# Performance work log

Hardware: AMD Instinct MI355X
Metric: run time of the kernel (lower is better)

The kernel has to match this reference:

```python
import jax, jax.numpy as jnp
import numpy as np

N_NODES = 50000
N_EDGES = 600000
CLASSIC_DIM = 128
GRAPH_OUTPUT_DIM = 96
NUM_RELATIONS = 4


def setup_inputs() -> dict:
    key = jax.random.key(0)
    ks = jax.random.split(key, 10)
    x = jax.random.normal(ks[0], (N_NODES, CLASSIC_DIM), dtype=jnp.float32)
    edge_index = jax.random.randint(ks[1], (2, N_EDGES), 0, N_NODES, dtype=jnp.int64)
    edge_type = jax.random.randint(ks[2], (N_EDGES,), 0, NUM_RELATIONS, dtype=jnp.int64)
    s1 = 1.0 / np.sqrt(CLASSIC_DIM)
    W_root1 = jax.random.normal(ks[3], (CLASSIC_DIM, CLASSIC_DIM), dtype=jnp.float32) * s1
    W_rel1 = jax.random.normal(ks[4], (NUM_RELATIONS, CLASSIC_DIM, CLASSIC_DIM), dtype=jnp.float32) * s1
    b1 = jnp.zeros((CLASSIC_DIM,), dtype=jnp.float32)
    W_root2 = jax.random.normal(ks[5], (CLASSIC_DIM, GRAPH_OUTPUT_DIM), dtype=jnp.float32) * s1
    W_rel2 = jax.random.normal(ks[6], (NUM_RELATIONS, CLASSIC_DIM, GRAPH_OUTPUT_DIM), dtype=jnp.float32) * s1
    b2 = jnp.zeros((GRAPH_OUTPUT_DIM,), dtype=jnp.float32)
    return {"classic_features": x, "edge_index": edge_index, "edge_type": edge_type,
            "W_root1": W_root1, "W_rel1": W_rel1, "b1": b1,
            "W_root2": W_root2, "W_rel2": W_rel2, "b2": b2}


def _rgcn_layer(x, edge_index, edge_type, W_root, W_rel, b):
    # RGCN: h_i = W_root x_i + b + sum_r (1/deg_{i,r}) * W_r * sum_{j in N_r(i)} x_j
    # Aggregate-then-transform (valid by linearity) to keep the matmul small.
    src, dst = edge_index[0], edge_index[1]
    msgs = x[src]  # [E, d_in] irregular gather
    out = x @ W_root + b
    n = x.shape[0]
    num_rel = W_rel.shape[0]
    for r in range(num_rel):  # small fixed loop over relation types
        mask = (edge_type == r).astype(x.dtype)  # [E]
        agg = jax.ops.segment_sum(msgs * mask[:, None], dst, num_segments=n)  # [N, d_in]
        deg = jax.ops.segment_sum(mask, dst, num_segments=n)  # [N]
        agg = agg / jnp.maximum(deg, 1.0)[:, None]  # mean per relation (PyG default norm)
        out = out + agg @ W_rel[r]
    return out


def reference(classic_features, edge_index, edge_type, W_root1, W_rel1, b1, W_root2, W_rel2, b2):
    h = _rgcn_layer(classic_features, edge_index, edge_type, W_root1, W_rel1, b1)
    h = jax.nn.relu(h)
    # dropout(0.2) is identity in eval mode
    out = _rgcn_layer(h, edge_index, edge_type, W_root2, W_rel2, b2)
    return out
```

## Files before the change

### kernel.cpp

```cpp
#include <hip/hip_runtime.h>

#define DIM_IN 128
#define NREL 4
#define KTOT (DIM_IN + NREL * DIM_IN)
#define CAP 32

typedef __attribute__((ext_vector_type(8))) short short8;
typedef __attribute__((ext_vector_type(4))) float floatx4;

__device__ inline unsigned short f2bf(float f) {
    union { float f; unsigned int i; } c;
    c.f = f;
    unsigned int r = c.i + 0x7FFF + ((c.i >> 16) & 1);
    return (unsigned short)(r >> 16);
}
__device__ inline float bf2f(unsigned short u) {
    union { unsigned int i; float f; } c;
    c.i = ((unsigned int)u) << 16;
    return c.f;
}

__device__ inline void gload16_lds(const void* g, void* l) {
    __builtin_amdgcn_global_load_lds((const __attribute__((address_space(1))) unsigned int*)g,
                                     (__attribute__((address_space(3))) unsigned int*)l,
                                     16, 0, 0);
}

__global__ __launch_bounds__(256) void prep_kernel(
    const float* __restrict__ x, unsigned short* __restrict__ xb, int n4,
    const float* __restrict__ Wroot1, const float* __restrict__ Wrel1,
    unsigned short* __restrict__ Wt1,
    const float* __restrict__ Wroot2, const float* __restrict__ Wrel2,
    unsigned short* __restrict__ Wt2,
    const int* __restrict__ ei, const int* __restrict__ et,
    int* __restrict__ counts, unsigned short* __restrict__ bucket, int E) {
    int t = blockIdx.x * 256 + threadIdx.x;
    if (t < E) {
        int b = ei[E + t] * NREL + et[t];
        int slot = atomicAdd(&counts[b], 1);
        if (slot < CAP) bucket[(size_t)b * CAP + slot] = (unsigned short)ei[t];
    }
    if (t < n4) {
        float4 v = ((const float4*)x)[t];
        ushort4 o;
        o.x = f2bf(v.x); o.y = f2bf(v.y); o.z = f2bf(v.z); o.w = f2bf(v.w);
        ((ushort4*)xb)[t] = o;
    }
    if (t < 128 * KTOT) {
        int n = t / KTOT, k = t - n * KTOT;
        float v = (k < DIM_IN) ? Wroot1[(size_t)k * 128 + n]
                               : Wrel1[(size_t)(k - DIM_IN) * 128 + n];
        Wt1[t] = f2bf(v);
    }
    if (t < 96 * KTOT) {
        int n = t / KTOT, k = t - n * KTOT;
        float v = (k < DIM_IN) ? Wroot2[(size_t)k * 96 + n]
                               : Wrel2[(size_t)(k - DIM_IN) * 96 + n];
        Wt2[t] = f2bf(v);
    }
}

__global__ __launch_bounds__(256) void agg_kernel(
    const unsigned short* __restrict__ feat, const unsigned short* __restrict__ bucket,
    const int* __restrict__ counts, unsigned short* __restrict__ agg, int nb) {
    int l16 = threadIdx.x & 15;
    int g = (blockIdx.x * 256 + threadIdx.x) >> 4;
    if (g >= nb) return;
    int cnt = counts[g];
    int m = (cnt < CAP) ? cnt : CAP;
    const unsigned short* bk = bucket + (size_t)g * CAP;
    float acc[8];
#pragma unroll
    for (int j = 0; j < 8; j++) acc[j] = 0.f;
    for (int base = 0; base < m; base += 16) {
        int mm = m - base;
        if (mm > 16) mm = 16;
        int pick = (l16 < mm) ? l16 : (mm - 1);
        int idx = bk[base + pick];
        for (int j = 0; j < mm; j++) {
            int s = __shfl(idx, j, 16);
            short8 u = *(const short8*)(feat + (size_t)s * DIM_IN + l16 * 8);
#pragma unroll
            for (int c = 0; c < 8; c++) acc[c] += bf2f((unsigned short)u[c]);
        }
    }
    float sc = (cnt > 0) ? (1.0f / (float)cnt) : 0.f;
    short8 o;
#pragma unroll
    for (int j = 0; j < 8; j++) o[j] = (short)f2bf(acc[j] * sc);
    *(short8*)(agg + (size_t)g * DIM_IN + l16 * 8) = o;
}

template <int NOUT, bool STORE_BF16_RELU>
__global__ __launch_bounds__(256) void mfma_gemm_kernel(
    const unsigned short* __restrict__ xb,
    const unsigned short* __restrict__ agg,
    const unsigned short* __restrict__ Wt,
    const float* __restrict__ bias,
    void* __restrict__ outp,
    int N) {
    constexpr int NT = NOUT / 32;
    constexpr int APAN = 64 * 32;
    constexpr int BPAN = NOUT * 32;
    __shared__ unsigned short sA[2 * APAN];
    __shared__ unsigned short sB[2 * BPAN];
    const int t = threadIdx.x;
    const int w = t >> 6;
    const int lane = t & 63;
    const int q = lane >> 4;
    const int l15 = lane & 15;
    const int wm = w >> 1, wn = w & 1;
    const int m0 = blockIdx.x * 64;

    floatx4 acc[2][NT];
#pragma unroll
    for (int mt = 0; mt < 2; mt++)
#pragma unroll
        for (int nt = 0; nt < NT; nt++) acc[mt][nt] = (floatx4)0.f;

    for (int ks = 0; ks < KTOT / 64; ks++) {
        const int k0 = ks * 64;
#pragma unroll
        for (int r = 0; r < 2; r++) {
            int idx = t + r * 256;
            int panel = idx >> 8;
            int rem = idx & 255;
            int row = rem >> 2, ch = rem & 3;
            int rowg = m0 + row;
            if (rowg >= N) rowg = N - 1;
            int col = panel * 32 + ch * 8;
            const unsigned short* gp =
                (k0 < DIM_IN)
                    ? (xb + (size_t)rowg * DIM_IN + k0 + col)
                    : (agg + (size_t)rowg * (NREL * DIM_IN) + (k0 - DIM_IN) + col);
            gload16_lds(gp, sA + (size_t)idx * 8);
        }
#pragma unroll
        for (int r = 0; r < (NOUT * 8) / 256; r++) {
            int idx = t + r * 256;
            int panel = idx / (NOUT * 4);
            int rem = idx - panel * (NOUT * 4);
            int nrow = rem >> 2, ch = rem & 3;
            gload16_lds(Wt + (size_t)nrow * KTOT + k0 + panel * 32 + ch * 8,
                        sB + (size_t)idx * 8);
        }
        __syncthreads();
#pragma unroll
        for (int s = 0; s < 2; s++) {
            short8 aF[2], bF[NT];
#pragma unroll
            for (int mt = 0; mt < 2; mt++)
                aF[mt] = *(const short8*)(sA + s * APAN +
                                          (size_t)(wm * 32 + mt * 16 + l15) * 32 + q * 8);
#pragma unroll
            for (int nt = 0; nt < NT; nt++)
                bF[nt] = *(const short8*)(sB + s * BPAN +
                                          (size_t)(wn * (NOUT / 2) + nt * 16 + l15) * 32 + q * 8);
#pragma unroll
            for (int mt = 0; mt < 2; mt++)
#pragma unroll
                for (int nt = 0; nt < NT; nt++)
                    acc[mt][nt] = __builtin_amdgcn_mfma_f32_16x16x32_bf16(aF[mt], bF[nt],
                                                                          acc[mt][nt], 0, 0, 0);
        }
        __syncthreads();
    }

#pragma unroll
    for (int nt = 0; nt < NT; nt++) {
        int colg = wn * (NOUT / 2) + nt * 16 + l15;
        float bv = bias[colg];
#pragma unroll
        for (int mt = 0; mt < 2; mt++) {
            int rbase = m0 + wm * 32 + mt * 16 + q * 4;
#pragma unroll
            for (int r = 0; r < 4; r++) {
                int grow = rbase + r;
                if (grow < N) {
                    float v = acc[mt][nt][r] + bv;
                    if (STORE_BF16_RELU) {
                        v = fmaxf(v, 0.f);
                        ((unsigned short*)outp)[(size_t)grow * NOUT + colg] = f2bf(v);
                    } else {
                        ((float*)outp)[(size_t)grow * NOUT + colg] = v;
                    }
                }
            }
        }
    }
}

extern "C" void kernel_launch(void* const* d_in, const int* in_sizes, int n_in,
                              void* d_out, int out_size, void* d_ws, size_t ws_size,
                              hipStream_t stream) {
    const float* x = (const float*)d_in[0];
    const int* ei = (const int*)d_in[1];
    const int* et = (const int*)d_in[2];
    const float* Wroot1 = (const float*)d_in[3];
    const float* Wrel1 = (const float*)d_in[4];
    const float* b1 = (const float*)d_in[5];
    const float* Wroot2 = (const float*)d_in[6];
    const float* Wrel2 = (const float*)d_in[7];
    const float* b2 = (const float*)d_in[8];
    float* out = (float*)d_out;

    int N = in_sizes[0] / DIM_IN;
    int E = in_sizes[2];
    int nb = N * NREL;

    char* p = (char*)d_ws;
    unsigned short* xb = (unsigned short*)p;     p += (size_t)N * DIM_IN * 2;
    unsigned short* hb = (unsigned short*)p;     p += (size_t)N * DIM_IN * 2;
    unsigned short* agg = (unsigned short*)p;    p += (size_t)nb * DIM_IN * 2;
    unsigned short* Wt1 = (unsigned short*)p;    p += (size_t)128 * KTOT * 2;
    unsigned short* Wt2 = (unsigned short*)p;    p += (size_t)96 * KTOT * 2;
    int* counts = (int*)p;                       p += (size_t)nb * 4;
    unsigned short* bucket = (unsigned short*)p; p += (size_t)nb * CAP * 2;
    if ((size_t)(p - (char*)d_ws) > ws_size) return;

    int n4 = N * DIM_IN / 4;
    int prepWork = n4;
    if (prepWork < E) prepWork = E;
    if (prepWork < 128 * KTOT) prepWork = 128 * KTOT;

    hipMemsetAsync(counts, 0, (size_t)nb * sizeof(int), stream);
    prep_kernel<<<(prepWork + 255) / 256, 256, 0, stream>>>(
        x, xb, n4, Wroot1, Wrel1, Wt1, Wroot2, Wrel2, Wt2, ei, et, counts, bucket, E);

    int gAgg = (nb * 16 + 255) / 256;
    int gB = (N + 63) / 64;
    agg_kernel<<<gAgg, 256, 0, stream>>>(xb, bucket, counts, agg, nb);
    mfma_gemm_kernel<128, true><<<gB, 256, 0, stream>>>(xb, agg, Wt1, b1, hb, N);
    agg_kernel<<<gAgg, 256, 0, stream>>>(hb, bucket, counts, agg, nb);
    mfma_gemm_kernel<96, false><<<gB, 256, 0, stream>>>(hb, agg, Wt2, b2, out, N);
}
```

Measured before the change: 228.8 us.

## Double-buffer A tiles in GEMM, load B from global, prefetch in aggregation

The GEMM now double-buffers the activation tile in shared memory, staging the next K-step while computing the current one. The weight fragments are read straight from global memory (they are small and cache-resident) instead of being staged through LDS. The aggregation kernel is software-pipelined so the next gathered row is loaded while the current one is accumulated. The aim is to hide global-load latency and cut LDS traffic and synchronisation, at the cost of more registers and uncoalesced weight reads from L2.

Result: slower. 266.0 us (+16.2%).

```diff
diff --git a/kernel.cpp b/kernel.cpp
--- a/kernel.cpp
+++ b/kernel.cpp
@@ -69,6 +69,7 @@
     int cnt = counts[g];
     int m = (cnt < CAP) ? cnt : CAP;
     const unsigned short* bk = bucket + (size_t)g * CAP;
+    const unsigned short* fb = feat + l16 * 8;
     float acc[8];
 #pragma unroll
     for (int j = 0; j < 8; j++) acc[j] = 0.f;
@@ -77,12 +78,17 @@
         if (mm > 16) mm = 16;
         int pick = (l16 < mm) ? l16 : (mm - 1);
         int idx = bk[base + pick];
-        for (int j = 0; j < mm; j++) {
-            int s = __shfl(idx, j, 16);
-            short8 u = *(const short8*)(feat + (size_t)s * DIM_IN + l16 * 8);
+        int s0 = __shfl(idx, 0, 16);
+        short8 u = *(const short8*)(fb + (size_t)s0 * DIM_IN);
+        for (int j = 1; j < mm; j++) {
+            int sn = __shfl(idx, j, 16);
+            short8 un = *(const short8*)(fb + (size_t)sn * DIM_IN);
 #pragma unroll
             for (int c = 0; c < 8; c++) acc[c] += bf2f((unsigned short)u[c]);
-        }
+            u = un;
+        }
+#pragma unroll
+        for (int c = 0; c < 8; c++) acc[c] += bf2f((unsigned short)u[c]);
     }
     float sc = (cnt > 0) ? (1.0f / (float)cnt) : 0.f;
     short8 o;
@@ -101,9 +107,8 @@
     int N) {
     constexpr int NT = NOUT / 32;
     constexpr int APAN = 64 * 32;
-    constexpr int BPAN = NOUT * 32;
-    __shared__ unsigned short sA[2 * APAN];
-    __shared__ unsigned short sB[2 * BPAN];
+    constexpr int KS = KTOT / 64;
+    __shared__ unsigned short sA[2][2 * APAN];
     const int t = threadIdx.x;
     const int w = t >> 6;
     const int lane = t & 63;
@@ -118,7 +123,9 @@
 #pragma unroll
         for (int nt = 0; nt < NT; nt++) acc[mt][nt] = (floatx4)0.f;
 
-    for (int ks = 0; ks < KTOT / 64; ks++) {
+    const unsigned short* WtB = Wt + (size_t)(wn * (NOUT / 2) + l15) * KTOT + q * 8;
+
+    auto stageA = [&](int ks, int buf) {
         const int k0 = ks * 64;
 #pragma unroll
         for (int r = 0; r < 2; r++) {
@@ -133,34 +140,34 @@
                 (k0 < DIM_IN)
                     ? (xb + (size_t)rowg * DIM_IN + k0 + col)
                     : (agg + (size_t)rowg * (NREL * DIM_IN) + (k0 - DIM_IN) + col);
-            gload16_lds(gp, sA + (size_t)idx * 8);
-        }
-#pragma unroll
-        for (int r = 0; r < (NOUT * 8) / 256; r++) {
-            int idx = t + r * 256;
-            int panel = idx / (NOUT * 4);
-            int rem = idx - panel * (NOUT * 4);
-            int nrow = rem >> 2, ch = rem & 3;
-            gload16_lds(Wt + (size_t)nrow * KTOT + k0 + panel * 32 + ch * 8,
-                        sB + (size_t)idx * 8);
-        }
-        __syncthreads();
+            gload16_lds(gp, &sA[buf][(size_t)idx * 8]);
+        }
+    };
+
+    stageA(0, 0);
+    __syncthreads();
+    for (int ks = 0; ks < KS; ks++) {
+        const int cur = ks & 1;
+        const int k0 = ks * 64;
+        short8 bF[2][NT];
+#pragma unroll
+        for (int s = 0; s < 2; s++)
+#pragma unroll
+            for (int nt = 0; nt < NT; nt++)
+                bF[s][nt] = *(const short8*)(WtB + (size_t)nt * 16 * KTOT + k0 + s * 32);
+        if (ks + 1 < KS) stageA(ks + 1, cur ^ 1);
 #pragma unroll
         for (int s = 0; s < 2; s++) {
-            short8 aF[2], bF[NT];
+            short8 aF[2];
 #pragma unroll
             for (int mt = 0; mt < 2; mt++)
-                aF[mt] = *(const short8*)(sA + s * APAN +
-                                          (size_t)(wm * 32 + mt * 16 + l15) * 32 + q * 8);
-#pragma unroll
-            for (int nt = 0; nt < NT; nt++)
-                bF[nt] = *(const short8*)(sB + s * BPAN +
-                                          (size_t)(wn * (NOUT / 2) + nt * 16 + l15) * 32 + q * 8);
+                aF[mt] = *(const short8*)(&sA[cur][(size_t)s * APAN +
+                                                   (size_t)(wm * 32 + mt * 16 + l15) * 32 + q * 8]);
 #pragma unroll
             for (int mt = 0; mt < 2; mt++)
 #pragma unroll
                 for (int nt = 0; nt < NT; nt++)
-                    acc[mt][nt] = __builtin_amdgcn_mfma_f32_16x16x32_bf16(aF[mt], bF[nt],
+                    acc[mt][nt] = __builtin_amdgcn_mfma_f32_16x16x32_bf16(aF[mt], bF[s][nt],
                                                                           acc[mt][nt], 0, 0, 0);
         }
         __syncthreads();
```
